# Kernel tuning notes

Measured on AMD Instinct MI355X. Metric: run time of the kernel, lower is better.

## Reference

```python
import jax, jax.numpy as jnp
import numpy as np
from jax import lax

B, T, P = 32, 4096, 64
IN, H = 2 * P, 256


def setup_inputs() -> dict:
    key = jax.random.key(0)
    ks = jax.random.split(key, 11)
    s_in = 1.0 / np.sqrt(H)  # torch nn.RNN init scale U(-1/sqrt(H), 1/sqrt(H))
    u = lambda k, shape: jax.random.uniform(k, shape, jnp.float32, -s_in, s_in)
    return {
        "input": jax.random.normal(ks[0], (B, T, IN), jnp.float32),
        "W_ih0": u(ks[1], (H, IN)), "W_hh0": u(ks[2], (H, H)),
        "b_ih0": u(ks[3], (H,)),   "b_hh0": u(ks[4], (H,)),
        "W_ih1": u(ks[5], (H, H)), "W_hh1": u(ks[6], (H, H)),
        "b_ih1": u(ks[7], (H,)),   "b_hh1": u(ks[8], (H,)),
        "fc_W": u(ks[9], (P, H)),  "fc_b": u(ks[10], (P,)),
    }


def _rnn_layer(x, W_ih, b_ih, W_hh, b_hh):
    # x: [B, T, C] -> out: [B, T, H]; h_t = tanh(x W_ih^T + b_ih + h W_hh^T + b_hh)
    pre = jnp.einsum('btc,hc->tbh', x, W_ih) + b_ih  # big GEMM hoisted out of scan

    def step(h, p):
        h = jnp.tanh(p + h @ W_hh.T + b_hh)
        return h, h

    h0 = jnp.zeros((x.shape[0], W_hh.shape[0]), x.dtype)
    _, ys = lax.scan(step, h0, pre)  # ys: [T, B, H]
    return jnp.transpose(ys, (1, 0, 2))


def reference(input, W_ih0, W_hh0, b_ih0, b_hh0, W_ih1, W_hh1, b_ih1, b_hh1, fc_W, fc_b):
    h1 = _rnn_layer(input, W_ih0, b_ih0, W_hh0, b_hh0)
    h2 = _rnn_layer(h1, W_ih1, b_ih1, W_hh1, b_hh1)
    flat = h2.reshape(-1, H)                     # [B*T, H]
    return jax.nn.sigmoid(flat @ fc_W.T + fc_b)  # [B*T, P]
```

## Files before the change

kernel.cpp:

```cpp
#include <hip/hip_runtime.h>

constexpr int Bsz = 32;
constexpr int T   = 4096;
constexpr int P   = 64;
constexpr int IN  = 128;
constexpr int H   = 256;
constexpr long M  = (long)Bsz * T;
constexpr int FS  = 16;
constexpr int C   = 16;
constexpr int NC  = T / C;
constexpr int RW  = 320;

__device__ int g_flags[3 * 32 * FS];

__global__ void zero_flags() {
  for (int i = threadIdx.x; i < 3 * 32 * FS; i += 256) g_flags[i] = 0;
}

template <int K>
__global__ __launch_bounds__(256) void gemm_pre(
    const float* __restrict__ X, const float* __restrict__ W,
    const float* __restrict__ b1, const float* __restrict__ b2,
    float* __restrict__ out) {
  constexpr int K4 = K / 4;
  __shared__ float4 a4[16][K4];
  __shared__ float  wch[256][33];
  const int tid = threadIdx.x;
  const long m0 = (long)blockIdx.x * 16;

  const float4* X4 = (const float4*)X;
#pragma unroll
  for (int i = 0; i < (16 * K4) / 256; ++i) {
    int idx = tid + 256 * i;
    int r = idx / K4, c = idx % K4;
    a4[r][c] = X4[(m0 + r) * K4 + c];
  }

  const int j = tid;
  const float bsum = b1[j] + b2[j];
  float acc[16];
#pragma unroll
  for (int r = 0; r < 16; ++r) acc[r] = 0.f;

  const float4* W4v = (const float4*)W;
  for (int kc = 0; kc < K4; kc += 8) {
    __syncthreads();
#pragma unroll
    for (int i = 0; i < 8; ++i) {
      int idx = tid + 256 * i;
      int jr = idx >> 3, c = idx & 7;
      float4 t4 = W4v[(long)jr * K4 + kc + c];
      wch[jr][4 * c + 0] = t4.x; wch[jr][4 * c + 1] = t4.y;
      wch[jr][4 * c + 2] = t4.z; wch[jr][4 * c + 3] = t4.w;
    }
    __syncthreads();
#pragma unroll
    for (int i4 = 0; i4 < 8; ++i4) {
      float wx = wch[j][4 * i4 + 0], wy = wch[j][4 * i4 + 1];
      float wz = wch[j][4 * i4 + 2], ww = wch[j][4 * i4 + 3];
#pragma unroll
      for (int r = 0; r < 16; ++r) {
        float4 av = a4[r][kc + i4];
        acc[r] += wx * av.x + wy * av.y + wz * av.z + ww * av.w;
      }
    }
  }
#pragma unroll
  for (int r = 0; r < 16; ++r)
    out[(m0 + r) * H + j] = acc[r] + bsum;
}

__device__ __forceinline__ float gload(const float* p) {
  return __hip_atomic_load(const_cast<float*>(p), __ATOMIC_RELAXED,
                           __HIP_MEMORY_SCOPE_AGENT);
}
__device__ __forceinline__ void gstore(float* p, float v) {
  __hip_atomic_store(p, v, __ATOMIC_RELAXED, __HIP_MEMORY_SCOPE_AGENT);
}
__device__ __forceinline__ void wait_ge(const int* f, int target, int& seen) {
  if (seen >= target) return;
  int v = __hip_atomic_load(const_cast<int*>(f), __ATOMIC_ACQUIRE,
                            __HIP_MEMORY_SCOPE_AGENT);
  while (v < target) {
    __builtin_amdgcn_s_sleep(8);
    v = __hip_atomic_load(const_cast<int*>(f), __ATOMIC_ACQUIRE,
                          __HIP_MEMORY_SCOPE_AGENT);
  }
  seen = v;
}
__device__ __forceinline__ void publish(int* f, int v) {
  __hip_atomic_store(f, v, __ATOMIC_RELEASE, __HIP_MEMORY_SCOPE_AGENT);
}

__device__ __forceinline__ void bar_lds() {
  asm volatile("s_waitcnt lgkmcnt(0)\n\ts_barrier" ::: "memory");
}
__device__ __forceinline__ void bar_full() {
  asm volatile("s_waitcnt vmcnt(0) lgkmcnt(0)\n\ts_barrier" ::: "memory");
}

__device__ __forceinline__ int padw(int c) { return (c >> 4) * 20 + (c & 15); }

struct WTile { float4 w[4][4]; };

__device__ __forceinline__ void load_wtile(const float* Wm, int wv, int jg,
                                           int ks, WTile& wt) {
  const float4* W4 = (const float4*)Wm;
#pragma unroll
  for (int r = 0; r < 4; ++r)
#pragma unroll
    for (int q = 0; q < 4; ++q)
      wt.w[r][q] = W4[(long)(wv * 16 + jg * 4 + r) * (H / 4) + ks * 4 + q];
#pragma unroll
  for (int r = 0; r < 4; ++r)
#pragma unroll
    for (int q = 0; q < 4; ++q)
      asm volatile("" : "+v"(wt.w[r][q].x), "+v"(wt.w[r][q].y),
                        "+v"(wt.w[r][q].z), "+v"(wt.w[r][q].w));
}

__device__ __forceinline__ float matvec_reduce(const WTile& wt, const float* hb,
                                               int bit4, int bit8) {
  float4 h0 = *(const float4*)(hb + 0);
  float4 h1 = *(const float4*)(hb + 4);
  float4 h2 = *(const float4*)(hb + 8);
  float4 h3 = *(const float4*)(hb + 12);
  float acc[4] = {0.f, 0.f, 0.f, 0.f};
#pragma unroll
  for (int r = 0; r < 4; ++r) {
    acc[r] += wt.w[r][0].x * h0.x + wt.w[r][0].y * h0.y +
              wt.w[r][0].z * h0.z + wt.w[r][0].w * h0.w;
    acc[r] += wt.w[r][1].x * h1.x + wt.w[r][1].y * h1.y +
              wt.w[r][1].z * h1.z + wt.w[r][1].w * h1.w;
    acc[r] += wt.w[r][2].x * h2.x + wt.w[r][2].y * h2.y +
              wt.w[r][2].z * h2.z + wt.w[r][2].w * h2.w;
    acc[r] += wt.w[r][3].x * h3.x + wt.w[r][3].y * h3.y +
              wt.w[r][3].z * h3.z + wt.w[r][3].w * h3.w;
  }
  __builtin_amdgcn_sched_barrier(0);
  float t0 = bit4 ? acc[0] : acc[2];
  float t1 = bit4 ? acc[1] : acc[3];
  float r0 = __int_as_float(__builtin_amdgcn_ds_swizzle(__float_as_int(t0), 0x101F));
  float r1 = __int_as_float(__builtin_amdgcn_ds_swizzle(__float_as_int(t1), 0x101F));
  float u0 = (bit4 ? acc[2] : acc[0]) + r0;
  float u1 = (bit4 ? acc[3] : acc[1]) + r1;
  float t2 = bit8 ? u0 : u1;
  float r2 = __int_as_float(__builtin_amdgcn_ds_swizzle(__float_as_int(t2), 0x201F));
  float s  = (bit8 ? u1 : u0) + r2;
  s += __int_as_float(__builtin_amdgcn_ds_swizzle(__float_as_int(s), 0x401F));
  s += __shfl_xor(s, 32, 64);
  return s;
}

template <bool ATOMPRE>
__device__ __forceinline__ void scan_role(
    const float* prebuf, const float* Wm, float* houtb,
    const int* inflag, int* outflag, int b,
    float (*ring)[C][RW], float (*hdb)[RW]) {
  const int tid = threadIdx.x, lane = tid & 63, wv = tid >> 6;
  const int jg = lane & 3, ks = lane >> 2;
  const int bit4 = lane & 4, bit8 = lane & 8;
  const int jj2 = ((lane >> 1) & 2) | ((lane >> 3) & 1);

  WTile wt; load_wtile(Wm, wv, jg, ks, wt);
  const int  jmine = wv * 16 + jg * 4 + jj2;
  const long base  = (long)b * T * H;
  float* houtj = houtb + base + jmine;
  const int wr  = wv * 20 + (jg * 4 + jj2);
  const int prd = padw(jmine);
  const int src = tid >> 8;
  const int sw  = padw(tid & 255);
  const int fr4 = (tid * 4) >> 8;
  const int fw4 = padw((tid * 4) & 255);

  if (tid < 2 * RW) ((float*)hdb)[tid] = 0.f;

  int seen = 0;
  if (ATOMPRE) {
    wait_ge(inflag, C, seen);
    float v0 = gload(prebuf + base + tid);
    float v1 = gload(prebuf + base + 1024 + tid);
    float v2 = gload(prebuf + base + 2048 + tid);
    float v3 = gload(prebuf + base + 3072 + tid);
    ring[0][src][sw] = v0;      ring[0][src + 4][sw] = v1;
    ring[0][src + 8][sw] = v2;  ring[0][src + 12][sw] = v3;
  } else {
    float4 v = ((const float4*)(prebuf + base))[tid];
    *(float4*)&ring[0][fr4][fw4] = v;
  }
  bar_full();

#pragma unroll 1
  for (int k = 0; k < NC; ++k) {
    const int kn = k + 1;
    const bool more = (kn < NC);
    float s0 = 0.f, s1 = 0.f, s2 = 0.f, s3 = 0.f;
    float4 sv = {0.f, 0.f, 0.f, 0.f};
    if (more) {
      const float* nb = prebuf + base + (long)kn * C * H;
      if (ATOMPRE) {
        wait_ge(inflag, (kn + 1) * C, seen);
        s0 = gload(nb + tid);        s1 = gload(nb + 1024 + tid);
        s2 = gload(nb + 2048 + tid); s3 = gload(nb + 3072 + tid);
      } else {
        sv = ((const float4*)nb)[tid];
      }
    }
#pragma unroll 2
    for (int r = 0; r < C; ++r) {
      const int t = k * C + r;
      float p = ring[k & 1][r][prd];
      float s = matvec_reduce(wt, hdb[r & 1] + ks * 20, bit4, bit8);
      float x = p + s;
      float e = __expf(2.f * x);
      float hn = 1.f - 2.f * __builtin_amdgcn_rcpf(e + 1.f);
      if (lane < 16) {
        hdb[(r + 1) & 1][wr] = hn;
        gstore(houtj + (long)t * H, hn);
      }
      if (r != C - 1) bar_lds();
    }
    if (more) {
      if (ATOMPRE) {
        ring[kn & 1][src][sw] = s0;      ring[kn & 1][src + 4][sw] = s1;
        ring[kn & 1][src + 8][sw] = s2;  ring[kn & 1][src + 12][sw] = s3;
      } else {
        *(float4*)&ring[kn & 1][fr4][fw4] = sv;
      }
    }
    bar_full();
    if (tid == 0) publish(outflag, kn * C);
  }
}

__device__ __forceinline__ void mid_role(
    const float* h1b, const float* Wm, const float* bi, const float* bh,
    float* pre2b, const int* Af, int* Mf, int b, float (*ring)[C][RW]) {
  const int tid = threadIdx.x, lane = tid & 63, wv = tid >> 6;
  const int jg = lane & 3, ks = lane >> 2;
  const int bit4 = lane & 4, bit8 = lane & 8;
  const int jj2 = ((lane >> 1) & 2) | ((lane >> 3) & 1);

  WTile wt; load_wtile(Wm, wv, jg, ks, wt);
  const int  jmine = wv * 16 + jg * 4 + jj2;
  const float bsum = bi[jmine] + bh[jmine];
  const long base  = (long)b * T * H;
  float* poutj = pre2b + base + jmine;
  const int src = tid >> 8, sw = padw(tid & 255);

  int seen = 0;
  wait_ge(Af, C, seen);
  {
    float v0 = gload(h1b + base + tid);
    float v1 = gload(h1b + base + 1024 + tid);
    float v2 = gload(h1b + base + 2048 + tid);
    float v3 = gload(h1b + base + 3072 + tid);
    ring[0][src][sw] = v0;      ring[0][src + 4][sw] = v1;
    ring[0][src + 8][sw] = v2;  ring[0][src + 12][sw] = v3;
  }
  bar_full();

#pragma unroll 1
  for (int k = 0; k < NC; ++k) {
    const int kn = k + 1;
    const bool more = (kn < NC);
    float s0 = 0.f, s1 = 0.f, s2 = 0.f, s3 = 0.f;
    if (more) {
      wait_ge(Af, (kn + 1) * C, seen);
      const float* nb = h1b + base + (long)kn * C * H;
      s0 = gload(nb + tid);        s1 = gload(nb + 1024 + tid);
      s2 = gload(nb + 2048 + tid); s3 = gload(nb + 3072 + tid);
    }
#pragma unroll 2
    for (int r = 0; r < C; ++r) {
      const int t = k * C + r;
      float s = matvec_reduce(wt, ring[k & 1][r] + ks * 20, bit4, bit8) + bsum;
      if (lane < 16) gstore(poutj + (long)t * H, s);
    }
    if (more) {
      ring[kn & 1][src][sw] = s0;      ring[kn & 1][src + 4][sw] = s1;
      ring[kn & 1][src + 8][sw] = s2;  ring[kn & 1][src + 12][sw] = s3;
    }
    bar_full();
    if (tid == 0) publish(Mf, kn * C);
  }
}

__device__ __forceinline__ void fc_role(
    const float* h2b, const float* fcWm, const float* fcbv, float* outp,
    const int* Bf, int b, float (*ring)[C][RW]) {
  const int tid = threadIdx.x, lane = tid & 63, wv = tid >> 6;
  const int jg = lane & 3, ks = lane >> 2;
  const int p = wv * 4 + jg;

  const float4* W4 = (const float4*)fcWm;
  float4 fw[4];
#pragma unroll
  for (int q = 0; q < 4; ++q) fw[q] = W4[(long)p * (H / 4) + ks * 4 + q];
  const float fb = fcbv[p];
  const long base  = (long)b * T * H;
  const long obase = (long)b * T * P;
  const int src = tid >> 8, sw = padw(tid & 255);

  int seen = 0;
  wait_ge(Bf, C, seen);
  {
    float v0 = gload(h2b + base + tid);
    float v1 = gload(h2b + base + 1024 + tid);
    float v2 = gload(h2b + base + 2048 + tid);
    float v3 = gload(h2b + base + 3072 + tid);
    ring[0][src][sw] = v0;      ring[0][src + 4][sw] = v1;
    ring[0][src + 8][sw] = v2;  ring[0][src + 12][sw] = v3;
  }
  bar_full();

#pragma unroll 1
  for (int k = 0; k < NC; ++k) {
    const int kn = k + 1;
    const bool more = (kn < NC);
    float s0 = 0.f, s1 = 0.f, s2 = 0.f, s3 = 0.f;
    if (more) {
      wait_ge(Bf, (kn + 1) * C, seen);
      const float* nb = h2b + base + (long)kn * C * H;
      s0 = gload(nb + tid);        s1 = gload(nb + 1024 + tid);
      s2 = gload(nb + 2048 + tid); s3 = gload(nb + 3072 + tid);
    }
#pragma unroll 2
    for (int r = 0; r < C; ++r) {
      const int t = k * C + r;
      const float* hb = ring[k & 1][r] + ks * 20;
      float4 h0 = *(const float4*)(hb + 0);
      float4 h1 = *(const float4*)(hb + 4);
      float4 h2 = *(const float4*)(hb + 8);
      float4 h3 = *(const float4*)(hb + 12);
      float s = fw[0].x * h0.x + fw[0].y * h0.y + fw[0].z * h0.z + fw[0].w * h0.w
              + fw[1].x * h1.x + fw[1].y * h1.y + fw[1].z * h1.z + fw[1].w * h1.w
              + fw[2].x * h2.x + fw[2].y * h2.y + fw[2].z * h2.z + fw[2].w * h2.w
              + fw[3].x * h3.x + fw[3].y * h3.y + fw[3].z * h3.z + fw[3].w * h3.w;
      s += __int_as_float(__builtin_amdgcn_ds_swizzle(__float_as_int(s), 0x101F));
      s += __int_as_float(__builtin_amdgcn_ds_swizzle(__float_as_int(s), 0x201F));
      s += __int_as_float(__builtin_amdgcn_ds_swizzle(__float_as_int(s), 0x401F));
      s += __shfl_xor(s, 32, 64);
      float xx = s + fb;
      float sig = __builtin_amdgcn_rcpf(1.f + __expf(-xx));
      if (lane < 4) outp[obase + (long)t * P + wv * 4 + lane] = sig;
    }
    if (more) {
      ring[kn & 1][src][sw] = s0;      ring[kn & 1][src + 4][sw] = s1;
      ring[kn & 1][src + 8][sw] = s2;  ring[kn & 1][src + 12][sw] = s3;
    }
    bar_full();
  }
}

__global__ __attribute__((amdgpu_flat_work_group_size(1024, 1024),
                          amdgpu_waves_per_eu(4, 4)))
void pipeline(float* bufPre, float* bufH,
              const float* __restrict__ W_hh0,
              const float* __restrict__ W_ih1,
              const float* __restrict__ b_ih1, const float* __restrict__ b_hh1,
              const float* __restrict__ W_hh1,
              const float* __restrict__ fcW, const float* __restrict__ fcb,
              float* __restrict__ outp) {
  __shared__ float ring[2][C][RW];
  __shared__ float hdb[2][RW];
  const int blk = blockIdx.x, role = blk >> 5, b = blk & 31;
  int* Af = g_flags + (0 * 32 + b) * FS;
  int* Mf = g_flags + (1 * 32 + b) * FS;
  int* Bf = g_flags + (2 * 32 + b) * FS;

  if (role == 0) {
    scan_role<false>(bufPre, W_hh0, bufH, nullptr, Af, b, ring, hdb);
  } else if (role == 1) {
    mid_role(bufH, W_ih1, b_ih1, b_hh1, bufPre, Af, Mf, b, ring);
  } else if (role == 2) {
    scan_role<true>(bufPre, W_hh1, bufH, Mf, Bf, b, ring, hdb);
  } else {
    fc_role(bufH, fcW, fcb, outp, Bf, b, ring);
  }
}

extern "C" void kernel_launch(void* const* d_in, const int* in_sizes, int n_in,
                              void* d_out, int out_size, void* d_ws, size_t ws_size,
                              hipStream_t stream) {
  const float* input = (const float*)d_in[0];
  const float* W_ih0 = (const float*)d_in[1];
  const float* W_hh0 = (const float*)d_in[2];
  const float* b_ih0 = (const float*)d_in[3];
  const float* b_hh0 = (const float*)d_in[4];
  const float* W_ih1 = (const float*)d_in[5];
  const float* W_hh1 = (const float*)d_in[6];
  const float* b_ih1 = (const float*)d_in[7];
  const float* b_hh1 = (const float*)d_in[8];
  const float* fc_W  = (const float*)d_in[9];
  const float* fc_b  = (const float*)d_in[10];
  float* out = (float*)d_out;

  float* bufPre = (float*)d_ws;
  float* bufH   = bufPre + (size_t)M * H;

  zero_flags<<<1, 256, 0, stream>>>();
  gemm_pre<IN><<<(int)(M / 16), 256, 0, stream>>>(input, W_ih0, b_ih0, b_hh0, bufPre);
  pipeline<<<128, 1024, 0, stream>>>(bufPre, bufH, W_hh0, W_ih1, b_ih1, b_hh1,
                                     W_hh1, fc_W, fc_b, out);
}
```

Measured before the change: 3.603 ms.

## Fuse input GEMM into pipeline and process two batches per block

The separate layer-0 input-projection GEMM kernel is removed and becomes a fifth producer role inside the persistent pipeline kernel, streaming per-chunk results to the layer-0 scan through flags. Each block now handles a pair of batch rows, interleaving two independent recurrences so one LDS barrier per timestep serves both, and the grid shrinks from 128 to 80 blocks. The chunk size is halved to tighten producer/consumer lag. The trade-off is a longer serial path per step and a 16-block GEMM role that may not keep ahead of the scan, while the kernel launch and the full pre-activation round trip no longer sit on the critical path.

```diff
diff --git a/kernel.cpp b/kernel.cpp
--- a/kernel.cpp
+++ b/kernel.cpp
@@ -7,67 +7,16 @@
 constexpr int H   = 256;
 constexpr long M  = (long)Bsz * T;
 constexpr int FS  = 16;
-constexpr int C   = 16;
+constexpr int C   = 8;
 constexpr int NC  = T / C;
 constexpr int RW  = 320;
-
-__device__ int g_flags[3 * 32 * FS];
+constexpr int XW  = 192;
+constexpr int NPAIR = 16;
+
+__device__ int g_flags[4 * NPAIR * FS];
 
 __global__ void zero_flags() {
-  for (int i = threadIdx.x; i < 3 * 32 * FS; i += 256) g_flags[i] = 0;
-}
-
-template <int K>
-__global__ __launch_bounds__(256) void gemm_pre(
-    const float* __restrict__ X, const float* __restrict__ W,
-    const float* __restrict__ b1, const float* __restrict__ b2,
-    float* __restrict__ out) {
-  constexpr int K4 = K / 4;
-  __shared__ float4 a4[16][K4];
-  __shared__ float  wch[256][33];
-  const int tid = threadIdx.x;
-  const long m0 = (long)blockIdx.x * 16;
-
-  const float4* X4 = (const float4*)X;
-#pragma unroll
-  for (int i = 0; i < (16 * K4) / 256; ++i) {
-    int idx = tid + 256 * i;
-    int r = idx / K4, c = idx % K4;
-    a4[r][c] = X4[(m0 + r) * K4 + c];
-  }
-
-  const int j = tid;
-  const float bsum = b1[j] + b2[j];
-  float acc[16];
-#pragma unroll
-  for (int r = 0; r < 16; ++r) acc[r] = 0.f;
-
-  const float4* W4v = (const float4*)W;
-  for (int kc = 0; kc < K4; kc += 8) {
-    __syncthreads();
-#pragma unroll
-    for (int i = 0; i < 8; ++i) {
-      int idx = tid + 256 * i;
-      int jr = idx >> 3, c = idx & 7;
-      float4 t4 = W4v[(long)jr * K4 + kc + c];
-      wch[jr][4 * c + 0] = t4.x; wch[jr][4 * c + 1] = t4.y;
-      wch[jr][4 * c + 2] = t4.z; wch[jr][4 * c + 3] = t4.w;
-    }
-    __syncthreads();
-#pragma unroll
-    for (int i4 = 0; i4 < 8; ++i4) {
-      float wx = wch[j][4 * i4 + 0], wy = wch[j][4 * i4 + 1];
-      float wz = wch[j][4 * i4 + 2], ww = wch[j][4 * i4 + 3];
-#pragma unroll
-      for (int r = 0; r < 16; ++r) {
-        float4 av = a4[r][kc + i4];
-        acc[r] += wx * av.x + wy * av.y + wz * av.z + ww * av.w;
-      }
-    }
-  }
-#pragma unroll
-  for (int r = 0; r < 16; ++r)
-    out[(m0 + r) * H + j] = acc[r] + bsum;
+  for (int i = threadIdx.x; i < 4 * NPAIR * FS; i += 256) g_flags[i] = 0;
 }
 
 __device__ __forceinline__ float gload(const float* p) {
@@ -100,6 +49,30 @@
 }
 
 __device__ __forceinline__ int padw(int c) { return (c >> 4) * 20 + (c & 15); }
+
+template <int PAT>
+__device__ __forceinline__ float swz(float x) {
+  return __int_as_float(__builtin_amdgcn_ds_swizzle(__float_as_int(x), PAT));
+}
+
+__device__ __forceinline__ float reduce16(const float acc[4], int bit4, int bit8) {
+  float t0 = bit4 ? acc[0] : acc[2];
+  float t1 = bit4 ? acc[1] : acc[3];
+  float r0 = swz<0x101F>(t0), r1 = swz<0x101F>(t1);
+  float u0 = (bit4 ? acc[2] : acc[0]) + r0;
+  float u1 = (bit4 ? acc[3] : acc[1]) + r1;
+  float t2 = bit8 ? u0 : u1;
+  float r2 = swz<0x201F>(t2);
+  float s  = (bit8 ? u1 : u0) + r2;
+  s += swz<0x401F>(s);
+  s += __shfl_xor(s, 32, 64);
+  return s;
+}
+
+__device__ __forceinline__ float tanh_f(float x) {
+  float e = __expf(2.f * x);
+  return 1.f - 2.f * __builtin_amdgcn_rcpf(e + 1.f);
+}
 
 struct WTile { float4 w[4][4]; };
 
@@ -138,104 +111,90 @@
               wt.w[r][3].z * h3.z + wt.w[r][3].w * h3.w;
   }
   __builtin_amdgcn_sched_barrier(0);
-  float t0 = bit4 ? acc[0] : acc[2];
-  float t1 = bit4 ? acc[1] : acc[3];
-  float r0 = __int_as_float(__builtin_amdgcn_ds_swizzle(__float_as_int(t0), 0x101F));
-  float r1 = __int_as_float(__builtin_amdgcn_ds_swizzle(__float_as_int(t1), 0x101F));
-  float u0 = (bit4 ? acc[2] : acc[0]) + r0;
-  float u1 = (bit4 ? acc[3] : acc[1]) + r1;
-  float t2 = bit8 ? u0 : u1;
-  float r2 = __int_as_float(__builtin_amdgcn_ds_swizzle(__float_as_int(t2), 0x201F));
-  float s  = (bit8 ? u1 : u0) + r2;
-  s += __int_as_float(__builtin_amdgcn_ds_swizzle(__float_as_int(s), 0x401F));
-  s += __shfl_xor(s, 32, 64);
-  return s;
-}
-
-template <bool ATOMPRE>
-__device__ __forceinline__ void scan_role(
-    const float* prebuf, const float* Wm, float* houtb,
-    const int* inflag, int* outflag, int b,
-    float (*ring)[C][RW], float (*hdb)[RW]) {
+  return reduce16(acc, bit4, bit8);
+}
+
+__device__ __forceinline__ void g_role(
+    const float* __restrict__ xin, const float* __restrict__ Wih,
+    const float* __restrict__ bi, const float* __restrict__ bh,
+    float* pre1b, int* Gf, int pr, float* pool) {
   const int tid = threadIdx.x, lane = tid & 63, wv = tid >> 6;
   const int jg = lane & 3, ks = lane >> 2;
   const int bit4 = lane & 4, bit8 = lane & 8;
   const int jj2 = ((lane >> 1) & 2) | ((lane >> 3) & 1);
 
-  WTile wt; load_wtile(Wm, wv, jg, ks, wt);
+  const float4* W4 = (const float4*)Wih;
+  float4 gwv[4][2];
+#pragma unroll
+  for (int r = 0; r < 4; ++r)
+#pragma unroll
+    for (int q = 0; q < 2; ++q)
+      gwv[r][q] = W4[(long)(wv * 16 + jg * 4 + r) * (IN / 4) + ks * 2 + q];
+
   const int  jmine = wv * 16 + jg * 4 + jj2;
-  const long base  = (long)b * T * H;
-  float* houtj = houtb + base + jmine;
-  const int wr  = wv * 20 + (jg * 4 + jj2);
-  const int prd = padw(jmine);
-  const int src = tid >> 8;
-  const int sw  = padw(tid & 255);
-  const int fr4 = (tid * 4) >> 8;
-  const int fw4 = padw((tid * 4) & 255);
-
-  if (tid < 2 * RW) ((float*)hdb)[tid] = 0.f;
-
-  int seen = 0;
-  if (ATOMPRE) {
-    wait_ge(inflag, C, seen);
-    float v0 = gload(prebuf + base + tid);
-    float v1 = gload(prebuf + base + 1024 + tid);
-    float v2 = gload(prebuf + base + 2048 + tid);
-    float v3 = gload(prebuf + base + 3072 + tid);
-    ring[0][src][sw] = v0;      ring[0][src + 4][sw] = v1;
-    ring[0][src + 8][sw] = v2;  ring[0][src + 12][sw] = v3;
-  } else {
-    float4 v = ((const float4*)(prebuf + base))[tid];
-    *(float4*)&ring[0][fr4][fw4] = v;
-  }
-  bar_full();
+  const float bsum = bi[jmine] + bh[jmine];
+  const long xb0 = (long)(2 * pr) * T * IN, xb1 = (long)(2 * pr + 1) * T * IN;
+  float* o0 = pre1b + (long)(2 * pr) * T * H + jmine;
+  float* o1 = pre1b + (long)(2 * pr + 1) * T * H + jmine;
+  const int gr = tid >> 7, gc = tid & 127;
+  const int gcw = (gc >> 3) * 12 + (gc & 7);
+  float* xrp = pool;
+
+  xrp[(0 * 2 + 0) * C * XW + gr * XW + gcw] = xin[xb0 + (long)gr * IN + gc];
+  xrp[(1 * 2 + 0) * C * XW + gr * XW + gcw] = xin[xb1 + (long)gr * IN + gc];
+  bar_lds();
 
 #pragma unroll 1
   for (int k = 0; k < NC; ++k) {
     const int kn = k + 1;
     const bool more = (kn < NC);
-    float s0 = 0.f, s1 = 0.f, s2 = 0.f, s3 = 0.f;
-    float4 sv = {0.f, 0.f, 0.f, 0.f};
-    if (more) {
-      const float* nb = prebuf + base + (long)kn * C * H;
-      if (ATOMPRE) {
-        wait_ge(inflag, (kn + 1) * C, seen);
-        s0 = gload(nb + tid);        s1 = gload(nb + 1024 + tid);
-        s2 = gload(nb + 2048 + tid); s3 = gload(nb + 3072 + tid);
-      } else {
-        sv = ((const float4*)nb)[tid];
-      }
-    }
+    float n0 = 0.f, n1 = 0.f;
+    if (more) {
+      n0 = xin[xb0 + ((long)kn * C + gr) * IN + gc];
+      n1 = xin[xb1 + ((long)kn * C + gr) * IN + gc];
+    }
+    const float* x0 = xrp + (0 * 2 + (k & 1)) * C * XW;
+    const float* x1 = xrp + (1 * 2 + (k & 1)) * C * XW;
 #pragma unroll 2
     for (int r = 0; r < C; ++r) {
       const int t = k * C + r;
-      float p = ring[k & 1][r][prd];
-      float s = matvec_reduce(wt, hdb[r & 1] + ks * 20, bit4, bit8);
-      float x = p + s;
-      float e = __expf(2.f * x);
-      float hn = 1.f - 2.f * __builtin_amdgcn_rcpf(e + 1.f);
+      const float* xa = x0 + r * XW + ks * 12;
+      float4 a0 = *(const float4*)(xa), a1 = *(const float4*)(xa + 4);
+      float acc[4];
+#pragma unroll
+      for (int r2 = 0; r2 < 4; ++r2)
+        acc[r2] = gwv[r2][0].x * a0.x + gwv[r2][0].y * a0.y +
+                  gwv[r2][0].z * a0.z + gwv[r2][0].w * a0.w +
+                  gwv[r2][1].x * a1.x + gwv[r2][1].y * a1.y +
+                  gwv[r2][1].z * a1.z + gwv[r2][1].w * a1.w;
+      float sA = reduce16(acc, bit4, bit8) + bsum;
+      const float* xc = x1 + r * XW + ks * 12;
+      float4 c0 = *(const float4*)(xc), c1 = *(const float4*)(xc + 4);
+      float acd[4];
+#pragma unroll
+      for (int r2 = 0; r2 < 4; ++r2)
+        acd[r2] = gwv[r2][0].x * c0.x + gwv[r2][0].y * c0.y +
+                  gwv[r2][0].z * c0.z + gwv[r2][0].w * c0.w +
+                  gwv[r2][1].x * c1.x + gwv[r2][1].y * c1.y +
+                  gwv[r2][1].z * c1.z + gwv[r2][1].w * c1.w;
+      float sB = reduce16(acd, bit4, bit8) + bsum;
       if (lane < 16) {
-        hdb[(r + 1) & 1][wr] = hn;
-        gstore(houtj + (long)t * H, hn);
+        gstore(o0 + (long)t * H, sA);
+        gstore(o1 + (long)t * H, sB);
       }
-      if (r != C - 1) bar_lds();
-    }
-    if (more) {
-      if (ATOMPRE) {
-        ring[kn & 1][src][sw] = s0;      ring[kn & 1][src + 4][sw] = s1;
-        ring[kn & 1][src + 8][sw] = s2;  ring[kn & 1][src + 12][sw] = s3;
-      } else {
-        *(float4*)&ring[kn & 1][fr4][fw4] = sv;
-      }
+    }
+    if (more) {
+      xrp[(0 * 2 + (kn & 1)) * C * XW + gr * XW + gcw] = n0;
+      xrp[(1 * 2 + (kn & 1)) * C * XW + gr * XW + gcw] = n1;
     }
     bar_full();
-    if (tid == 0) publish(outflag, kn * C);
-  }
-}
-
-__device__ __forceinline__ void mid_role(
-    const float* h1b, const float* Wm, const float* bi, const float* bh,
-    float* pre2b, const int* Af, int* Mf, int b, float (*ring)[C][RW]) {
+    if (tid == 0) publish(Gf, kn * C);
+  }
+}
+
+__device__ __forceinline__ void scan_role2(
+    const float* prebuf, const float* __restrict__ Wm, float* houtb,
+    const int* inflag, int* outflag, int pr, float* pool) {
   const int tid = threadIdx.x, lane = tid & 63, wv = tid >> 6;
   const int jg = lane & 3, ks = lane >> 2;
   const int bit4 = lane & 4, bit8 = lane & 8;
@@ -243,20 +202,31 @@
 
   WTile wt; load_wtile(Wm, wv, jg, ks, wt);
   const int  jmine = wv * 16 + jg * 4 + jj2;
-  const float bsum = bi[jmine] + bh[jmine];
-  const long base  = (long)b * T * H;
-  float* poutj = pre2b + base + jmine;
-  const int src = tid >> 8, sw = padw(tid & 255);
+  const long base0 = (long)(2 * pr) * T * H;
+  const long base1 = (long)(2 * pr + 1) * T * H;
+  float* ho0 = houtb + base0 + jmine;
+  float* ho1 = houtb + base1 + jmine;
+  const int wr  = wv * 20 + (jg * 4 + jj2);
+  const int prd = padw(jmine);
+  const int sr0 = tid >> 8;
+  const int sc  = padw(tid & 255);
+
+  float* ringp = pool;
+  float* hdbp  = pool + 2 * 2 * C * RW;
+
+  for (int i = tid; i < 4 * RW; i += 1024) hdbp[i] = 0.f;
 
   int seen = 0;
-  wait_ge(Af, C, seen);
+  wait_ge(inflag, C, seen);
   {
-    float v0 = gload(h1b + base + tid);
-    float v1 = gload(h1b + base + 1024 + tid);
-    float v2 = gload(h1b + base + 2048 + tid);
-    float v3 = gload(h1b + base + 3072 + tid);
-    ring[0][src][sw] = v0;      ring[0][src + 4][sw] = v1;
-    ring[0][src + 8][sw] = v2;  ring[0][src + 12][sw] = v3;
+    float a0 = gload(prebuf + base0 + tid);
+    float a1 = gload(prebuf + base0 + 1024 + tid);
+    float c0 = gload(prebuf + base1 + tid);
+    float c1 = gload(prebuf + base1 + 1024 + tid);
+    ringp[(0 * 2 + 0) * C * RW + sr0 * RW + sc] = a0;
+    ringp[(0 * 2 + 0) * C * RW + (sr0 + 4) * RW + sc] = a1;
+    ringp[(1 * 2 + 0) * C * RW + sr0 * RW + sc] = c0;
+    ringp[(1 * 2 + 0) * C * RW + (sr0 + 4) * RW + sc] = c1;
   }
   bar_full();
 
@@ -264,71 +234,166 @@
   for (int k = 0; k < NC; ++k) {
     const int kn = k + 1;
     const bool more = (kn < NC);
-    float s0 = 0.f, s1 = 0.f, s2 = 0.f, s3 = 0.f;
-    if (more) {
-      wait_ge(Af, (kn + 1) * C, seen);
-      const float* nb = h1b + base + (long)kn * C * H;
-      s0 = gload(nb + tid);        s1 = gload(nb + 1024 + tid);
-      s2 = gload(nb + 2048 + tid); s3 = gload(nb + 3072 + tid);
-    }
+    float s00 = 0.f, s01 = 0.f, s10 = 0.f, s11 = 0.f;
+    if (more) {
+      wait_ge(inflag, (kn + 1) * C, seen);
+      const float* n0 = prebuf + base0 + (long)kn * C * H;
+      const float* n1 = prebuf + base1 + (long)kn * C * H;
+      s00 = gload(n0 + tid); s01 = gload(n0 + 1024 + tid);
+      s10 = gload(n1 + tid); s11 = gload(n1 + 1024 + tid);
+    }
+    const float* rb0 = ringp + (0 * 2 + (k & 1)) * C * RW;
+    const float* rb1 = ringp + (1 * 2 + (k & 1)) * C * RW;
 #pragma unroll 2
     for (int r = 0; r < C; ++r) {
       const int t = k * C + r;
-      float s = matvec_reduce(wt, ring[k & 1][r] + ks * 20, bit4, bit8) + bsum;
-      if (lane < 16) gstore(poutj + (long)t * H, s);
-    }
-    if (more) {
-      ring[kn & 1][src][sw] = s0;      ring[kn & 1][src + 4][sw] = s1;
-      ring[kn & 1][src + 8][sw] = s2;  ring[kn & 1][src + 12][sw] = s3;
+      float p0 = rb0[r * RW + prd];
+      float p1 = rb1[r * RW + prd];
+      float sA = matvec_reduce(wt, hdbp + (0 * 2 + (r & 1)) * RW + ks * 20, bit4, bit8);
+      float hn0 = tanh_f(p0 + sA);
+      float sB = matvec_reduce(wt, hdbp + (1 * 2 + (r & 1)) * RW + ks * 20, bit4, bit8);
+      float hn1 = tanh_f(p1 + sB);
+      if (lane < 16) {
+        hdbp[(0 * 2 + ((r + 1) & 1)) * RW + wr] = hn0;
+        hdbp[(1 * 2 + ((r + 1) & 1)) * RW + wr] = hn1;
+        gstore(ho0 + (long)t * H, hn0);
+        gstore(ho1 + (long)t * H, hn1);
+      }
+      if (r != C - 1) bar_lds();
+    }
+    if (more) {
+      float* w0 = ringp + (0 * 2 + (kn & 1)) * C * RW;
+      float* w1 = ringp + (1 * 2 + (kn & 1)) * C * RW;
+      w0[sr0 * RW + sc] = s00; w0[(sr0 + 4) * RW + sc] = s01;
+      w1[sr0 * RW + sc] = s10; w1[(sr0 + 4) * RW + sc] = s11;
     }
     bar_full();
-    if (tid == 0) publish(Mf, kn * C);
-  }
-}
-
-__device__ __forceinline__ void fc_role(
-    const float* h2b, const float* fcWm, const float* fcbv, float* outp,
-    const int* Bf, int b, float (*ring)[C][RW]) {
+    if (tid == 0) publish(outflag, kn * C);
+  }
+}
+
+__device__ __forceinline__ void mid_role2(
+    const float* h1b, const float* __restrict__ Wm,
+    const float* __restrict__ bi, const float* __restrict__ bh,
+    float* pre2b, const int* Af, int* Mf, int pr, float* pool) {
   const int tid = threadIdx.x, lane = tid & 63, wv = tid >> 6;
   const int jg = lane & 3, ks = lane >> 2;
-  const int p = wv * 4 + jg;
-
-  const float4* W4 = (const float4*)fcWm;
-  float4 fw[4];
-#pragma unroll
-  for (int q = 0; q < 4; ++q) fw[q] = W4[(long)p * (H / 4) + ks * 4 + q];
-  const float fb = fcbv[p];
-  const long base  = (long)b * T * H;
-  const long obase = (long)b * T * P;
-  const int src = tid >> 8, sw = padw(tid & 255);
+  const int bit4 = lane & 4, bit8 = lane & 8;
+  const int jj2 = ((lane >> 1) & 2) | ((lane >> 3) & 1);
+
+  WTile wt; load_wtile(Wm, wv, jg, ks, wt);
+  const int  jmine = wv * 16 + jg * 4 + jj2;
+  const float bsum = bi[jmine] + bh[jmine];
+  const long base0 = (long)(2 * pr) * T * H;
+  const long base1 = (long)(2 * pr + 1) * T * H;
+  float* o0 = pre2b + base0 + jmine;
+  float* o1 = pre2b + base1 + jmine;
+  const int sr0 = tid >> 8;
+  const int sc  = padw(tid & 255);
+  float* ringp = pool;
 
   int seen = 0;
-  wait_ge(Bf, C, seen);
+  wait_ge(Af, C, seen);
   {
-    float v0 = gload(h2b + base + tid);
-    float v1 = gload(h2b + base + 1024 + tid);
-    float v2 = gload(h2b + base + 2048 + tid);
-    float v3 = gload(h2b + base + 3072 + tid);
-    ring[0][src][sw] = v0;      ring[0][src + 4][sw] = v1;
-    ring[0][src + 8][sw] = v2;  ring[0][src + 12][sw] = v3;
-  }
-  bar_full();
+    float a0 = gload(h1b + base0 + tid);
+    float a1 = gload(h1b + base0 + 1024 + tid);
+    float c0 = gload(h1b + base1 + tid);
+    float c1 = gload(h1b + base1 + 1024 + tid);
+    ringp[(0 * 2 + 0) * C * RW + sr0 * RW + sc] = a0;
+    ringp[(0 * 2 + 0) * C * RW + (sr0 + 4) * RW + sc] = a1;
+    ringp[(1 * 2 + 0) * C * RW + sr0 * RW + sc] = c0;
+    ringp[(1 * 2 + 0) * C * RW + (sr0 + 4) * RW + sc] = c1;
+  }
+  bar_lds();
 
 #pragma unroll 1
   for (int k = 0; k < NC; ++k) {
     const int kn = k + 1;
     const bool more = (kn < NC);
-    float s0 = 0.f, s1 = 0.f, s2 = 0.f, s3 = 0.f;
-    if (more) {
-      wait_ge(Bf, (kn + 1) * C, seen);
-      const float* nb = h2b + base + (long)kn * C * H;
-      s0 = gload(nb + tid);        s1 = gload(nb + 1024 + tid);
-      s2 = gload(nb + 2048 + tid); s3 = gload(nb + 3072 + tid);
-    }
+    float s00 = 0.f, s01 = 0.f, s10 = 0.f, s11 = 0.f;
+    if (more) {
+      wait_ge(Af, (kn + 1) * C, seen);
+      const float* n0 = h1b + base0 + (long)kn * C * H;
+      const float* n1 = h1b + base1 + (long)kn * C * H;
+      s00 = gload(n0 + tid); s01 = gload(n0 + 1024 + tid);
+      s10 = gload(n1 + tid); s11 = gload(n1 + 1024 + tid);
+    }
+    const float* rb0 = ringp + (0 * 2 + (k & 1)) * C * RW;
+    const float* rb1 = ringp + (1 * 2 + (k & 1)) * C * RW;
 #pragma unroll 2
     for (int r = 0; r < C; ++r) {
       const int t = k * C + r;
-      const float* hb = ring[k & 1][r] + ks * 20;
+      float sA = matvec_reduce(wt, rb0 + r * RW + ks * 20, bit4, bit8) + bsum;
+      float sB = matvec_reduce(wt, rb1 + r * RW + ks * 20, bit4, bit8) + bsum;
+      if (lane < 16) {
+        gstore(o0 + (long)t * H, sA);
+        gstore(o1 + (long)t * H, sB);
+      }
+    }
+    if (more) {
+      float* w0 = ringp + (0 * 2 + (kn & 1)) * C * RW;
+      float* w1 = ringp + (1 * 2 + (kn & 1)) * C * RW;
+      w0[sr0 * RW + sc] = s00; w0[(sr0 + 4) * RW + sc] = s01;
+      w1[sr0 * RW + sc] = s10; w1[(sr0 + 4) * RW + sc] = s11;
+    }
+    bar_full();
+    if (tid == 0) publish(Mf, kn * C);
+  }
+}
+
+__device__ __forceinline__ void fc_role2(
+    const float* h2b, const float* __restrict__ fcWm,
+    const float* __restrict__ fcbv, float* __restrict__ outp,
+    const int* Bf, int pr, float* pool) {
+  const int tid = threadIdx.x, lane = tid & 63, wv = tid >> 6;
+  const int jg = lane & 3, ks = lane >> 2;
+  const int p = wv * 4 + jg;
+
+  const float4* W4 = (const float4*)fcWm;
+  float4 fw[4];
+#pragma unroll
+  for (int q = 0; q < 4; ++q) fw[q] = W4[(long)p * (H / 4) + ks * 4 + q];
+  const float fb = fcbv[p];
+  const long base0 = (long)(2 * pr) * T * H;
+  const long base1 = (long)(2 * pr + 1) * T * H;
+  const long ob0 = (long)(2 * pr) * T * P;
+  const long ob1 = (long)(2 * pr + 1) * T * P;
+  const int sr0 = tid >> 8;
+  const int sc  = padw(tid & 255);
+  float* ringp = pool;
+
+  int seen = 0;
+  wait_ge(Bf, C, seen);
+  {
+    float a0 = gload(h2b + base0 + tid);
+    float a1 = gload(h2b + base0 + 1024 + tid);
+    float c0 = gload(h2b + base1 + tid);
+    float c1 = gload(h2b + base1 + 1024 + tid);
+    ringp[(0 * 2 + 0) * C * RW + sr0 * RW + sc] = a0;
+    ringp[(0 * 2 + 0) * C * RW + (sr0 + 4) * RW + sc] = a1;
+    ringp[(1 * 2 + 0) * C * RW + sr0 * RW + sc] = c0;
+    ringp[(1 * 2 + 0) * C * RW + (sr0 + 4) * RW + sc] = c1;
+  }
+  bar_lds();
+
+#pragma unroll 1
+  for (int k = 0; k < NC; ++k) {
+    const int kn = k + 1;
+    const bool more = (kn < NC);
+    float s00 = 0.f, s01 = 0.f, s10 = 0.f, s11 = 0.f;
+    if (more) {
+      wait_ge(Bf, (kn + 1) * C, seen);
+      const float* n0 = h2b + base0 + (long)kn * C * H;
+      const float* n1 = h2b + base1 + (long)kn * C * H;
+      s00 = gload(n0 + tid); s01 = gload(n0 + 1024 + tid);
+      s10 = gload(n1 + tid); s11 = gload(n1 + 1024 + tid);
+    }
+    const float* rb0 = ringp + (0 * 2 + (k & 1)) * C * RW;
+    const float* rb1 = ringp + (1 * 2 + (k & 1)) * C * RW;
+#pragma unroll 2
+    for (int r = 0; r < C; ++r) {
+      const int t = k * C + r;
+      const float* hb = rb0 + r * RW + ks * 20;
       float4 h0 = *(const float4*)(hb + 0);
       float4 h1 = *(const float4*)(hb + 4);
       float4 h2 = *(const float4*)(hb + 8);
@@ -337,46 +402,64 @@
               + fw[1].x * h1.x + fw[1].y * h1.y + fw[1].z * h1.z + fw[1].w * h1.w
               + fw[2].x * h2.x + fw[2].y * h2.y + fw[2].z * h2.z + fw[2].w * h2.w
               + fw[3].x * h3.x + fw[3].y * h3.y + fw[3].z * h3.z + fw[3].w * h3.w;
-      s += __int_as_float(__builtin_amdgcn_ds_swizzle(__float_as_int(s), 0x101F));
-      s += __int_as_float(__builtin_amdgcn_ds_swizzle(__float_as_int(s), 0x201F));
-      s += __int_as_float(__builtin_amdgcn_ds_swizzle(__float_as_int(s), 0x401F));
+      s += swz<0x101F>(s); s += swz<0x201F>(s); s += swz<0x401F>(s);
       s += __shfl_xor(s, 32, 64);
-      float xx = s + fb;
-      float sig = __builtin_amdgcn_rcpf(1.f + __expf(-xx));
-      if (lane < 4) outp[obase + (long)t * P + wv * 4 + lane] = sig;
-    }
-    if (more) {
-      ring[kn & 1][src][sw] = s0;      ring[kn & 1][src + 4][sw] = s1;
-      ring[kn & 1][src + 8][sw] = s2;  ring[kn & 1][src + 12][sw] = s3;
-    }
-    bar_full();
+      float sig0 = __builtin_amdgcn_rcpf(1.f + __expf(-(s + fb)));
+
+      const float* hc = rb1 + r * RW + ks * 20;
+      float4 g0 = *(const float4*)(hc + 0);
+      float4 g1 = *(const float4*)(hc + 4);
+      float4 g2 = *(const float4*)(hc + 8);
+      float4 g3 = *(const float4*)(hc + 12);
+      float u = fw[0].x * g0.x + fw[0].y * g0.y + fw[0].z * g0.z + fw[0].w * g0.w
+              + fw[1].x * g1.x + fw[1].y * g1.y + fw[1].z * g1.z + fw[1].w * g1.w
+              + fw[2].x * g2.x + fw[2].y * g2.y + fw[2].z * g2.z + fw[2].w * g2.w
+              + fw[3].x * g3.x + fw[3].y * g3.y + fw[3].z * g3.z + fw[3].w * g3.w;
+      u += swz<0x101F>(u); u += swz<0x201F>(u); u += swz<0x401F>(u);
+      u += __shfl_xor(u, 32, 64);
+      float sig1 = __builtin_amdgcn_rcpf(1.f + __expf(-(u + fb)));
+
+      if (lane < 4) {
+        outp[ob0 + (long)t * P + wv * 4 + lane] = sig0;
+        outp[ob1 + (long)t * P + wv * 4 + lane] = sig1;
+      }
+    }
+    if (more) {
+      float* w0 = ringp + (0 * 2 + (kn & 1)) * C * RW;
+      float* w1 = ringp + (1 * 2 + (kn & 1)) * C * RW;
+      w0[sr0 * RW + sc] = s00; w0[(sr0 + 4) * RW + sc] = s01;
+      w1[sr0 * RW + sc] = s10; w1[(sr0 + 4) * RW + sc] = s11;
+    }
+    bar_lds();
   }
 }
 
 __global__ __attribute__((amdgpu_flat_work_group_size(1024, 1024),
                           amdgpu_waves_per_eu(4, 4)))
-void pipeline(float* bufPre, float* bufH,
-              const float* __restrict__ W_hh0,
-              const float* __restrict__ W_ih1,
-              const float* __restrict__ b_ih1, const float* __restrict__ b_hh1,
-              const float* __restrict__ W_hh1,
+void pipeline(const float* __restrict__ input, float* bufPre, float* bufH,
+              const float* __restrict__ W_ih0, const float* __restrict__ b_ih0,
+              const float* __restrict__ b_hh0, const float* __restrict__ W_hh0,
+              const float* __restrict__ W_ih1, const float* __restrict__ b_ih1,
+              const float* __restrict__ b_hh1, const float* __restrict__ W_hh1,
               const float* __restrict__ fcW, const float* __restrict__ fcb,
               float* __restrict__ outp) {
-  __shared__ float ring[2][C][RW];
-  __shared__ float hdb[2][RW];
-  const int blk = blockIdx.x, role = blk >> 5, b = blk & 31;
-  int* Af = g_flags + (0 * 32 + b) * FS;
-  int* Mf = g_flags + (1 * 32 + b) * FS;
-  int* Bf = g_flags + (2 * 32 + b) * FS;
+  __shared__ float pool[2 * 2 * C * RW + 2 * 2 * RW];
+  const int blk = blockIdx.x, role = blk >> 4, pr = blk & 15;
+  int* Gf = g_flags + (0 * NPAIR + pr) * FS;
+  int* Af = g_flags + (1 * NPAIR + pr) * FS;
+  int* Mf = g_flags + (2 * NPAIR + pr) * FS;
+  int* Bf = g_flags + (3 * NPAIR + pr) * FS;
 
   if (role == 0) {
-    scan_role<false>(bufPre, W_hh0, bufH, nullptr, Af, b, ring, hdb);
+    g_role(input, W_ih0, b_ih0, b_hh0, bufPre, Gf, pr, pool);
   } else if (role == 1) {
-    mid_role(bufH, W_ih1, b_ih1, b_hh1, bufPre, Af, Mf, b, ring);
+    scan_role2(bufPre, W_hh0, bufH, Gf, Af, pr, pool);
   } else if (role == 2) {
-    scan_role<true>(bufPre, W_hh1, bufH, Mf, Bf, b, ring, hdb);
+    mid_role2(bufH, W_ih1, b_ih1, b_hh1, bufPre, Af, Mf, pr, pool);
+  } else if (role == 3) {
+    scan_role2(bufPre, W_hh1, bufH, Mf, Bf, pr, pool);
   } else {
-    fc_role(bufH, fcW, fcb, outp, Bf, b, ring);
+    fc_role2(bufH, fcW, fcb, outp, Bf, pr, pool);
   }
 }
 
@@ -400,7 +483,7 @@
   float* bufH   = bufPre + (size_t)M * H;
 
   zero_flags<<<1, 256, 0, stream>>>();
-  gemm_pre<IN><<<(int)(M / 16), 256, 0, stream>>>(input, W_ih0, b_ih0, b_hh0, bufPre);
-  pipeline<<<128, 1024, 0, stream>>>(bufPre, bufH, W_hh0, W_ih1, b_ih1, b_hh1,
-                                     W_hh1, fc_W, fc_b, out);
-}
+  pipeline<<<5 * NPAIR, 1024, 0, stream>>>(
+      input, bufPre, bufH, W_ih0, b_ih0, b_hh0, W_hh0,
+      W_ih1, b_ih1, b_hh1, W_hh1, fc_W, fc_b, out);
+}
```

Measured after the change: 5.544 ms. 1.54x slower.
